# Optimization experiments

Hardware: AMD Instinct MI355X
Metric: run time of the kernel (lower is better)

Reference implementation:

```python
import jax, jax.numpy as jnp
import numpy as np

DELTA = 0.5  # EMA coefficient from __init__
B, N, CAT, FEAT, K = 8, 32768, 128, 128, 64


def setup_inputs() -> dict:
    key = jax.random.key(0)
    k1, k2 = jax.random.split(key)
    inp = jax.random.normal(k1, (B, N, CAT), dtype=jnp.float32)
    # nn.init.constant(weight, 1/sqrt(in_features))
    weight = jnp.full((CAT, FEAT), 1.0 / np.sqrt(FEAT), dtype=jnp.float32)
    keys = jnp.arange(K, dtype=jnp.int32)  # unique feat_dict keys, in [0, category)
    values = jax.random.normal(k2, (K, FEAT), dtype=jnp.float32)
    return {"input": inp, "weight": weight, "keys": keys, "values": values}


def reference(input, weight, keys, values):
    # output = (input @ weight).permute(0, 2, 1): (B, N, CAT) x (CAT, FEAT) -> (B, FEAT, N)
    output = jnp.einsum('bnc,cf->bfn', input, weight)
    # Per-key EMA update followed by scalar-L2-norm row overwrite (faithful to
    # torch: weight[key] = ||delta*w_k + (1-delta)*v_k||_2 broadcast over the row).
    new_rows = DELTA * weight[keys] + (1.0 - DELTA) * values           # (K, FEAT)
    norms = jnp.sqrt(jnp.sum(new_rows * new_rows, axis=1, keepdims=True))  # (K, 1)
    new_weight = weight.at[keys].set(jnp.broadcast_to(norms, new_rows.shape))
    return output, new_weight
```

## Files before the change

### kernel.cpp

```cpp
#include <hip/hip_runtime.h>
#include <math.h>

constexpr int B_ = 8, N_ = 32768, CAT_ = 128, FEAT_ = 128, K_ = 64;
constexpr float DELTA_ = 0.5f;

typedef __bf16 bf16x8 __attribute__((ext_vector_type(8)));
typedef float f32x4 __attribute__((ext_vector_type(4)));

constexpr int BLOCK = 512;
constexpr int NPB   = 256;
constexpr int GEMM_BLOCKS = (B_ * N_) / NPB;

__global__ void prep_kernel(const float* __restrict__ weight,
                            const int* __restrict__ keys,
                            const float* __restrict__ values,
                            float* __restrict__ outw,
                            __bf16* __restrict__ wTs)
{
    const int r = blockIdx.x;
    const int t = threadIdx.x;
    float w = weight[r * FEAT_ + t];
    wTs[t * CAT_ + (r ^ ((t & 7) << 3))] = (__bf16)w;

    bool keyed = false;
    for (int i = 0; i < K_; ++i) keyed |= (keys[i] == r);
    if (!keyed) outw[r * FEAT_ + t] = w;

    if (r < K_ && t < 64) {
        const int key = keys[r];
        float a0 = DELTA_ * weight[key * FEAT_ + t]      + (1.0f - DELTA_) * values[r * FEAT_ + t];
        float a1 = DELTA_ * weight[key * FEAT_ + t + 64] + (1.0f - DELTA_) * values[r * FEAT_ + t + 64];
        float ss = a0 * a0 + a1 * a1;
        #pragma unroll
        for (int off = 32; off > 0; off >>= 1)
            ss += __shfl_down(ss, off, 64);
        float nrm = sqrtf(__shfl(ss, 0, 64));
        outw[key * FEAT_ + t]      = nrm;
        outw[key * FEAT_ + t + 64] = nrm;
    }
}

__global__ __launch_bounds__(BLOCK, 4) void gemm_kernel(
    const float* __restrict__ input,
    const __bf16* __restrict__ wTs,
    float* __restrict__ out)
{
    __shared__ __bf16 wt[FEAT_ * CAT_];

    const int tid  = threadIdx.x;
    const int wid  = tid >> 6;
    const int lane = tid & 63;

    #pragma unroll
    for (int j = 0; j < 4; ++j) {
        int off = j * 8192 + wid * 1024;
        __builtin_amdgcn_global_load_lds(
            (const __attribute__((address_space(1))) void*)((const char*)wTs + off + lane * 16),
            (__attribute__((address_space(3))) void*)((char*)wt + off),
            16, 0, 0);
    }

    const int qlo = lane & 15;
    const int qhi = lane >> 4;
    const int bid = blockIdx.x;
    const int b   = bid >> 7;
    const int nb  = bid & 127;
    const int n0  = nb * NPB + wid * 32;

    f32x4 acc[8][2];
    #pragma unroll
    for (int i = 0; i < 8; ++i)
        #pragma unroll
        for (int j = 0; j < 2; ++j)
            acc[i][j] = (f32x4)0.0f;

    const float* in_base = input + ((size_t)b * N_ + n0) * CAT_;

    __syncthreads();

    #pragma unroll
    for (int ck = 0; ck < 4; ++ck) {
        bf16x8 bfrag[2];
        #pragma unroll
        for (int nt = 0; nt < 2; ++nt) {
            const float* p = in_base + (size_t)(nt * 16 + qlo) * CAT_ + ck * 32 + qhi * 8;
            f32x4 v0 = *(const f32x4*)p;
            f32x4 v1 = *(const f32x4*)(p + 4);
            bf16x8 t;
            #pragma unroll
            for (int e = 0; e < 4; ++e) {
                t[e]     = (__bf16)v0[e];
                t[e + 4] = (__bf16)v1[e];
            }
            bfrag[nt] = t;
        }
        const int cswz = (ck * 32 + qhi * 8) ^ ((qlo & 7) << 3);
        #pragma unroll
        for (int mt = 0; mt < 8; ++mt) {
            bf16x8 af = *(const bf16x8*)&wt[(mt * 16 + qlo) * CAT_ + cswz];
            acc[mt][0] = __builtin_amdgcn_mfma_f32_16x16x32_bf16(af, bfrag[0], acc[mt][0], 0, 0, 0);
            acc[mt][1] = __builtin_amdgcn_mfma_f32_16x16x32_bf16(af, bfrag[1], acc[mt][1], 0, 0, 0);
        }
    }

    float* outp = out + (size_t)b * FEAT_ * N_ + n0;
    #pragma unroll
    for (int mt = 0; mt < 8; ++mt) {
        #pragma unroll
        for (int nt = 0; nt < 2; ++nt) {
            #pragma unroll
            for (int r = 0; r < 4; ++r) {
                int f = mt * 16 + qhi * 4 + r;
                outp[(size_t)f * N_ + nt * 16 + qlo] = acc[mt][nt][r];
            }
        }
    }
}

constexpr int LDSTR = 136;
constexpr int FB_BLOCKS = (B_ * N_) / 128;

__global__ __launch_bounds__(256, 4) void ocm_fused(
    const float* __restrict__ input,
    const float* __restrict__ weight,
    const int* __restrict__ keys,
    const float* __restrict__ values,
    float* __restrict__ out)
{
    const int bid = blockIdx.x;
    const int tid = threadIdx.x;

    if (bid >= FB_BLOCKS) {
        float* outw = out + (size_t)B_ * FEAT_ * N_;
        const int r = bid - FB_BLOCKS;
        bool keyed = false;
        for (int i = 0; i < K_; ++i) keyed |= (keys[i] == r);
        if (!keyed && tid < FEAT_)
            outw[r * FEAT_ + tid] = weight[r * FEAT_ + tid];
        if (r < K_ && tid < 64) {
            const int key = keys[r];
            float a0 = DELTA_ * weight[key * FEAT_ + tid]      + (1.0f - DELTA_) * values[r * FEAT_ + tid];
            float a1 = DELTA_ * weight[key * FEAT_ + tid + 64] + (1.0f - DELTA_) * values[r * FEAT_ + tid + 64];
            float ss = a0 * a0 + a1 * a1;
            #pragma unroll
            for (int off = 32; off > 0; off >>= 1)
                ss += __shfl_down(ss, off, 64);
            float nrm = sqrtf(__shfl(ss, 0, 64));
            outw[key * FEAT_ + tid]      = nrm;
            outw[key * FEAT_ + tid + 64] = nrm;
        }
        return;
    }

    __shared__ __bf16 wt[FEAT_ * LDSTR];
    #pragma unroll
    for (int j = 0; j < (CAT_ * FEAT_) / 256; ++j) {
        int i = tid + j * 256;
        int c = i >> 7;
        int f = i & (FEAT_ - 1);
        wt[f * LDSTR + c] = (__bf16)weight[i];
    }
    __syncthreads();

    const int wid  = tid >> 6;
    const int lane = tid & 63;
    const int qlo  = lane & 15;
    const int qhi  = lane >> 4;
    const int b    = bid >> 8;
    const int nb   = bid & 255;
    const int n0   = nb * 128 + wid * 32;

    f32x4 acc[8][2];
    #pragma unroll
    for (int i = 0; i < 8; ++i)
        #pragma unroll
        for (int j = 0; j < 2; ++j)
            acc[i][j] = (f32x4)0.0f;

    const float* in_base = input + ((size_t)b * N_ + n0) * CAT_;

    #pragma unroll
    for (int ck = 0; ck < 4; ++ck) {
        bf16x8 bfrag[2];
        #pragma unroll
        for (int nt = 0; nt < 2; ++nt) {
            const float* p = in_base + (size_t)(nt * 16 + qlo) * CAT_ + ck * 32 + qhi * 8;
            f32x4 v0 = *(const f32x4*)p;
            f32x4 v1 = *(const f32x4*)(p + 4);
            bf16x8 t;
            t[0] = (__bf16)v0[0]; t[1] = (__bf16)v0[1]; t[2] = (__bf16)v0[2]; t[3] = (__bf16)v0[3];
            t[4] = (__bf16)v1[0]; t[5] = (__bf16)v1[1]; t[6] = (__bf16)v1[2]; t[7] = (__bf16)v1[3];
            bfrag[nt] = t;
        }
        #pragma unroll
        for (int mt = 0; mt < 8; ++mt) {
            bf16x8 afrag = *(const bf16x8*)&wt[(mt * 16 + qlo) * LDSTR + ck * 32 + qhi * 8];
            acc[mt][0] = __builtin_amdgcn_mfma_f32_16x16x32_bf16(afrag, bfrag[0], acc[mt][0], 0, 0, 0);
            acc[mt][1] = __builtin_amdgcn_mfma_f32_16x16x32_bf16(afrag, bfrag[1], acc[mt][1], 0, 0, 0);
        }
    }

    float* outp = out + (size_t)b * FEAT_ * N_ + n0;
    #pragma unroll
    for (int mt = 0; mt < 8; ++mt) {
        #pragma unroll
        for (int nt = 0; nt < 2; ++nt) {
            #pragma unroll
            for (int r = 0; r < 4; ++r) {
                int f = mt * 16 + qhi * 4 + r;
                outp[(size_t)f * N_ + nt * 16 + qlo] = acc[mt][nt][r];
            }
        }
    }
}

extern "C" void kernel_launch(void* const* d_in, const int* in_sizes, int n_in,
                              void* d_out, int out_size, void* d_ws, size_t ws_size,
                              hipStream_t stream) {
    const float* input  = (const float*)d_in[0];
    const float* weight = (const float*)d_in[1];
    const int*   keys   = (const int*)d_in[2];
    const float* values = (const float*)d_in[3];
    float* out = (float*)d_out;

    if (ws_size >= (size_t)CAT_ * FEAT_ * sizeof(__bf16)) {
        __bf16* wTs = (__bf16*)d_ws;
        float* outw = out + (size_t)B_ * FEAT_ * N_;
        prep_kernel<<<CAT_, FEAT_, 0, stream>>>(weight, keys, values, outw, wTs);
        gemm_kernel<<<GEMM_BLOCKS, BLOCK, 0, stream>>>(input, wTs, out);
    } else {
        ocm_fused<<<FB_BLOCKS + CAT_, 256, 0, stream>>>(input, weight, keys, values, out);
    }
}
```

Measured before the change: 53.77 us.

## Switch GEMM to 32x32x16 MFMA tiles with nontemporal output stores

```diff
diff --git a/kernel.cpp b/kernel.cpp
--- a/kernel.cpp
+++ b/kernel.cpp
@@ -6,6 +6,7 @@
 
 typedef __bf16 bf16x8 __attribute__((ext_vector_type(8)));
 typedef float f32x4 __attribute__((ext_vector_type(4)));
+typedef float f32x16 __attribute__((ext_vector_type(16)));
 
 constexpr int BLOCK = 512;
 constexpr int NPB   = 256;
@@ -40,7 +41,7 @@
     }
 }
 
-__global__ __launch_bounds__(BLOCK, 4) void gemm_kernel(
+__global__ __launch_bounds__(BLOCK, 2) void gemm_kernel(
     const float* __restrict__ input,
     const __bf16* __restrict__ wTs,
     float* __restrict__ out)
@@ -60,59 +61,48 @@
             16, 0, 0);
     }
 
-    const int qlo = lane & 15;
-    const int qhi = lane >> 4;
+    const int nl = lane & 31;
+    const int kg = lane >> 5;
     const int bid = blockIdx.x;
     const int b   = bid >> 7;
     const int nb  = bid & 127;
     const int n0  = nb * NPB + wid * 32;
 
-    f32x4 acc[8][2];
-    #pragma unroll
-    for (int i = 0; i < 8; ++i)
-        #pragma unroll
-        for (int j = 0; j < 2; ++j)
-            acc[i][j] = (f32x4)0.0f;
-
-    const float* in_base = input + ((size_t)b * N_ + n0) * CAT_;
+    f32x16 acc[4];
+    #pragma unroll
+    for (int i = 0; i < 4; ++i)
+        acc[i] = (f32x16)0.0f;
+
+    const float* inp = input + ((size_t)b * N_ + n0 + nl) * CAT_;
 
     __syncthreads();
 
     #pragma unroll
-    for (int ck = 0; ck < 4; ++ck) {
-        bf16x8 bfrag[2];
-        #pragma unroll
-        for (int nt = 0; nt < 2; ++nt) {
-            const float* p = in_base + (size_t)(nt * 16 + qlo) * CAT_ + ck * 32 + qhi * 8;
-            f32x4 v0 = *(const f32x4*)p;
-            f32x4 v1 = *(const f32x4*)(p + 4);
-            bf16x8 t;
-            #pragma unroll
-            for (int e = 0; e < 4; ++e) {
-                t[e]     = (__bf16)v0[e];
-                t[e + 4] = (__bf16)v1[e];
-            }
-            bfrag[nt] = t;
-        }
-        const int cswz = (ck * 32 + qhi * 8) ^ ((qlo & 7) << 3);
-        #pragma unroll
-        for (int mt = 0; mt < 8; ++mt) {
-            bf16x8 af = *(const bf16x8*)&wt[(mt * 16 + qlo) * CAT_ + cswz];
-            acc[mt][0] = __builtin_amdgcn_mfma_f32_16x16x32_bf16(af, bfrag[0], acc[mt][0], 0, 0, 0);
-            acc[mt][1] = __builtin_amdgcn_mfma_f32_16x16x32_bf16(af, bfrag[1], acc[mt][1], 0, 0, 0);
-        }
-    }
-
-    float* outp = out + (size_t)b * FEAT_ * N_ + n0;
-    #pragma unroll
-    for (int mt = 0; mt < 8; ++mt) {
-        #pragma unroll
-        for (int nt = 0; nt < 2; ++nt) {
-            #pragma unroll
-            for (int r = 0; r < 4; ++r) {
-                int f = mt * 16 + qhi * 4 + r;
-                outp[(size_t)f * N_ + nt * 16 + qlo] = acc[mt][nt][r];
-            }
+    for (int ck = 0; ck < 8; ++ck) {
+        const int c0 = ck * 16 + kg * 8;
+        f32x4 v0 = *(const f32x4*)(inp + c0);
+        f32x4 v1 = *(const f32x4*)(inp + c0 + 4);
+        bf16x8 bfrag;
+        #pragma unroll
+        for (int e = 0; e < 4; ++e) {
+            bfrag[e]     = (__bf16)v0[e];
+            bfrag[e + 4] = (__bf16)v1[e];
+        }
+        #pragma unroll
+        for (int mt = 0; mt < 4; ++mt) {
+            const int f = mt * 32 + nl;
+            bf16x8 af = *(const bf16x8*)&wt[f * CAT_ + (c0 ^ ((f & 7) << 3))];
+            acc[mt] = __builtin_amdgcn_mfma_f32_32x32x16_bf16(af, bfrag, acc[mt], 0, 0, 0);
+        }
+    }
+
+    float* outp = out + (size_t)b * FEAT_ * N_ + n0 + nl;
+    #pragma unroll
+    for (int mt = 0; mt < 4; ++mt) {
+        #pragma unroll
+        for (int r = 0; r < 16; ++r) {
+            const int f = mt * 32 + (r & 3) + 8 * (r >> 2) + 4 * kg;
+            __builtin_nontemporal_store(acc[mt][r], outp + (size_t)f * N_);
         }
     }
 }
```

Result: faster. 51.87 us (-3.5%).
